# Performance work log

Measured on AMD Instinct MI355X. Metric: run time of the kernel, lower is better.

The kernel has to match this reference:

```python
import jax, jax.numpy as jnp
import numpy as np

N_NODES = 100000
N_EDGES = 1600000
NEG_SLOPE = 0.2  # DGL GATConv default leaky_relu slope
BN_EPS = 1e-5


def setup_inputs() -> dict:
    key = jax.random.key(0)
    ks = jax.random.split(key, 10)
    feats = jax.random.normal(ks[0], (N_NODES, 128), dtype=jnp.float32)
    src = jax.random.randint(ks[1], (N_EDGES,), 0, N_NODES, dtype=jnp.int64)
    dst = jax.random.randint(ks[2], (N_EDGES,), 0, N_NODES, dtype=jnp.int64)
    fc_w = jax.random.normal(ks[3], (256, 128), dtype=jnp.float32) * 0.05   # H*D x in_feats
    attn_l = jax.random.normal(ks[4], (4, 64), dtype=jnp.float32) * 0.05
    attn_r = jax.random.normal(ks[5], (4, 64), dtype=jnp.float32) * 0.05
    res_w = jax.random.normal(ks[6], (256, 128), dtype=jnp.float32) * 0.05  # residual projection
    bias = jax.random.normal(ks[7], (4, 64), dtype=jnp.float32) * 0.05
    gamma = jnp.ones((64,), dtype=jnp.float32)
    beta = jnp.zeros((64,), dtype=jnp.float32)
    return {"feats": feats, "src": src, "dst": dst, "fc_w": fc_w,
            "attn_l": attn_l, "attn_r": attn_r, "res_w": res_w,
            "bias": bias, "gamma": gamma, "beta": beta}


def reference(feats, src, dst, fc_w, attn_l, attn_r, res_w, bias, gamma, beta):
    N = feats.shape[0]
    H, D = attn_l.shape
    # projected features [N, H, D] (feat_drop is identity in eval mode)
    h = (feats @ fc_w.T).reshape(N, H, D)
    # per-node attention logits [N, H]
    el = jnp.sum(h * attn_l[None], axis=-1)
    er = jnp.sum(h * attn_r[None], axis=-1)
    # edge logits, leaky relu
    e = el[src] + er[dst]                       # [E, H]
    e = jnp.where(e > 0, e, NEG_SLOPE * e)
    # numerically stable segment softmax over incoming edges of each dst node
    m = jax.ops.segment_max(e, dst, num_segments=N)       # [N, H]
    ex = jnp.exp(e - m[dst])                               # [E, H]
    s = jax.ops.segment_sum(ex, dst, num_segments=N)       # [N, H]
    alpha = ex / s[dst]                                    # [E, H]
    # weighted message aggregation: scatter-add alpha * h_src into dst
    msg = h[src] * alpha[:, :, None]                       # [E, H, D]
    rst = jax.ops.segment_sum(msg, dst, num_segments=N)    # [N, H, D]
    # residual projection + bias + activation (elu)
    res = (feats @ res_w.T).reshape(N, H, D)
    rst = jax.nn.elu(rst + res + bias[None])
    # mean over heads -> [N, D]
    out = rst.mean(axis=1)
    # BatchNorm1d (training stats: biased variance over the node/batch axis)
    mu = out.mean(axis=0)
    var = out.var(axis=0)
    return (out - mu) * jax.lax.rsqrt(var + BN_EPS) * gamma + beta
```

## Files before the change

### kernel.cpp

```cpp
#include <hip/hip_runtime.h>

#define N_NODES 100000
#define N_PAD   100096
#define N_EDGES 1600000
#define NEG_SLOPE 0.2f
#define BN_EPS 1e-5f

typedef __attribute__((ext_vector_type(8))) short short8;
typedef __attribute__((ext_vector_type(4))) float floatx4;

static const size_t OFF_AB   = 0;
static const size_t OFF_BB   = 25624576;
static const size_t OFF_H    = 25755648;
static const size_t OFF_RES  = 76955648;
static const size_t OFF_EL   = 128155648;
static const size_t OFF_ER   = 129755648;
static const size_t OFF_DEG  = 131355648;
static const size_t OFF_RS   = 131755648;
static const size_t OFF_CUR  = 132155664;
static const size_t OFF_ESRC = 132555664;
static const size_t OFF_BS   = 138955664;
static const size_t OFF_BN   = 138956176;

__device__ __forceinline__ unsigned short f2bf(float x) {
  unsigned int u = __float_as_uint(x);
  unsigned int r = (u + 0x7fffu + ((u >> 16) & 1u)) >> 16;
  return (unsigned short)r;
}
__device__ __forceinline__ float bf2f(unsigned short u) {
  return __uint_as_float(((unsigned int)u) << 16);
}

__global__ __launch_bounds__(256) void k_pre(
    const float* __restrict__ feats, const float* __restrict__ fc_w,
    const float* __restrict__ res_w, const int* __restrict__ dst,
    unsigned short* __restrict__ Ab, unsigned short* __restrict__ Bb,
    int* __restrict__ deg)
{
  const int b = blockIdx.x;
  if (b < 6256) {
    int c = b * 256 + threadIdx.x;
    int r = c >> 4, j = c & 15;
    unsigned short v[8];
    if (r < N_NODES) {
      const float* p = feats + (size_t)r * 128 + j * 8;
      float4 a = *(const float4*)p, bb = *(const float4*)(p + 4);
      v[0]=f2bf(a.x); v[1]=f2bf(a.y); v[2]=f2bf(a.z); v[3]=f2bf(a.w);
      v[4]=f2bf(bb.x); v[5]=f2bf(bb.y); v[6]=f2bf(bb.z); v[7]=f2bf(bb.w);
    } else {
      for (int i = 0; i < 8; i++) v[i] = 0;
    }
    size_t idx = (size_t)(r >> 7) * 2048 + ((r >> 4) & 7) * 256 + (j >> 2) * 64
               + (r & 15) + 16 * (j & 3);
    *(short8*)(Ab + idx * 8) = *(short8*)v;
  } else if (b < 12506) {
    int e = (b - 6256) * 256 + threadIdx.x;
    if (e < N_EDGES) atomicAdd(&deg[dst[e]], 1);
  } else {
    int c = (b - 12506) * 256 + threadIdx.x;
    int n = c >> 4, j = c & 15;
    const float* W = (n < 256) ? (fc_w + (size_t)n * 128) : (res_w + (size_t)(n - 256) * 128);
    const float* p = W + j * 8;
    float4 a = *(const float4*)p, bb = *(const float4*)(p + 4);
    unsigned short v[8];
    v[0]=f2bf(a.x); v[1]=f2bf(a.y); v[2]=f2bf(a.z); v[3]=f2bf(a.w);
    v[4]=f2bf(bb.x); v[5]=f2bf(bb.y); v[6]=f2bf(bb.z); v[7]=f2bf(bb.w);
    size_t idx = (size_t)(n >> 7) * 2048 + ((n >> 4) & 7) * 256 + (j >> 2) * 64
               + (n & 15) + 16 * (j & 3);
    *(short8*)(Bb + idx * 8) = *(short8*)v;
  }
}

__global__ __launch_bounds__(256) void k_mm(
    const unsigned short* __restrict__ Ab, const unsigned short* __restrict__ Bb,
    const float* __restrict__ bias, const float* __restrict__ attn_l,
    const float* __restrict__ attn_r,
    unsigned short* __restrict__ hbuf, unsigned short* __restrict__ resbuf,
    float* __restrict__ el, float* __restrict__ er)
{
  __shared__ unsigned short sA[16384];
  const int tid = threadIdx.x;
  const int w = tid >> 6, L = tid & 63;
  const int blk = blockIdx.x, nb = blockIdx.y;

  {
    const unsigned short* ga = Ab + (size_t)blk * 16384;
    #pragma unroll
    for (int i = 0; i < 8; i++) {
      int off = (i * 256 + w * 64) * 8;
      __builtin_amdgcn_global_load_lds(
          (const __attribute__((address_space(1))) unsigned int*)(ga + off + L * 8),
          (__attribute__((address_space(3))) unsigned int*)(sA + off),
          16, 0, 0);
    }
  }
  const int mh = w & 1, nh = w >> 1;
  floatx4 acc[4][4] = {};
  __syncthreads();

  const unsigned short* gb = Bb + ((size_t)nb * 2048 + nh * 4 * 256) * 8 + L * 8;
  #pragma unroll
  for (int s = 0; s < 4; s++) {
    short8 a[4], b[4];
    #pragma unroll
    for (int t = 0; t < 4; t++)
      a[t] = *(const short8*)(sA + ((mh * 4 + t) * 256 + s * 64 + L) * 8);
    #pragma unroll
    for (int t = 0; t < 4; t++)
      b[t] = *(const short8*)(gb + ((size_t)t * 256 + s * 64) * 8);
    #pragma unroll
    for (int mt = 0; mt < 4; mt++)
      #pragma unroll
      for (int nt = 0; nt < 4; nt++)
        acc[mt][nt] = __builtin_amdgcn_mfma_f32_16x16x32_bf16(a[mt], b[nt], acc[mt][nt], 0, 0, 0);
  }

  const int q = L >> 4, cn = L & 15;
  const int r0 = blk * 128 + mh * 64;
  if (nb < 2) {
    const int head = nb * 2 + nh;
    const int col0 = nb * 128 + nh * 64;
    float al[4], ar[4];
    #pragma unroll
    for (int nt = 0; nt < 4; nt++) {
      al[nt] = attn_l[head * 64 + nt * 16 + cn];
      ar[nt] = attn_r[head * 64 + nt * 16 + cn];
    }
    #pragma unroll
    for (int mt = 0; mt < 4; mt++)
      #pragma unroll
      for (int r = 0; r < 4; r++) {
        const int row = r0 + mt * 16 + q * 4 + r;
        float pl = 0.f, pr = 0.f;
        #pragma unroll
        for (int nt = 0; nt < 4; nt++) {
          pl = fmaf(acc[mt][nt][r], al[nt], pl);
          pr = fmaf(acc[mt][nt][r], ar[nt], pr);
        }
        #pragma unroll
        for (int o = 1; o < 16; o <<= 1) {
          pl += __shfl_xor(pl, o, 64);
          pr += __shfl_xor(pr, o, 64);
        }
        if (row < N_NODES) {
          #pragma unroll
          for (int nt = 0; nt < 4; nt++)
            hbuf[(size_t)row * 256 + col0 + nt * 16 + cn] = f2bf(acc[mt][nt][r]);
          if (cn == 0) {
            el[row * 4 + head] = pl;
            er[row * 4 + head] = pr;
          }
        }
      }
  } else {
    const int rc0 = (nb - 2) * 128 + nh * 64;
    #pragma unroll
    for (int mt = 0; mt < 4; mt++)
      #pragma unroll
      for (int r = 0; r < 4; r++) {
        const int row = r0 + mt * 16 + q * 4 + r;
        if (row < N_NODES)
          #pragma unroll
          for (int nt = 0; nt < 4; nt++) {
            float v = acc[mt][nt][r] + bias[rc0 + nt * 16 + cn];
            resbuf[(size_t)row * 256 + rc0 + nt * 16 + cn] = f2bf(v);
          }
      }
  }
}

__global__ __launch_bounds__(256) void k_scan1(const int* __restrict__ deg,
                                               int* __restrict__ rs, int* __restrict__ bsums)
{
  __shared__ int tmp[256];
  const int t = threadIdx.x;
  const int base = blockIdx.x * 1024 + t * 4;
  int v0 = 0, v1 = 0, v2 = 0, v3 = 0;
  if (base + 0 < N_NODES) v0 = deg[base + 0];
  if (base + 1 < N_NODES) v1 = deg[base + 1];
  if (base + 2 < N_NODES) v2 = deg[base + 2];
  if (base + 3 < N_NODES) v3 = deg[base + 3];
  const int tsum = v0 + v1 + v2 + v3;
  tmp[t] = tsum;
  __syncthreads();
  for (int o = 1; o < 256; o <<= 1) {
    int x = (t >= o) ? tmp[t - o] : 0;
    __syncthreads();
    tmp[t] += x;
    __syncthreads();
  }
  const int excl = tmp[t] - tsum;
  if (base + 0 < N_NODES) rs[base + 0] = excl;
  if (base + 1 < N_NODES) rs[base + 1] = excl + v0;
  if (base + 2 < N_NODES) rs[base + 2] = excl + v0 + v1;
  if (base + 3 < N_NODES) rs[base + 3] = excl + v0 + v1 + v2;
  if (t == 255) bsums[blockIdx.x] = tmp[t];
}

__global__ __launch_bounds__(256) void k_scan3(int* __restrict__ rs,
                                               const int* __restrict__ bsums,
                                               int* __restrict__ cursor)
{
  __shared__ int sb[128];
  const int t = threadIdx.x;
  int raw = 0;
  if (t < 128) { raw = (t < 98) ? bsums[t] : 0; sb[t] = raw; }
  __syncthreads();
  for (int o = 1; o < 128; o <<= 1) {
    int x = (t >= o && t < 128) ? sb[t - o] : 0;
    __syncthreads();
    if (t < 128) sb[t] += x;
    __syncthreads();
  }
  if (t < 128) sb[t] -= raw;
  __syncthreads();
  const int i = blockIdx.x * 256 + t;
  if (i < N_NODES) {
    int v = rs[i] + sb[i >> 10];
    rs[i] = v;
    cursor[i] = v;
  } else if (i == N_NODES) {
    rs[N_NODES] = N_EDGES;
  }
}

__global__ __launch_bounds__(256) void k_scatter(const int* __restrict__ src,
                                                 const int* __restrict__ dst,
                                                 int* __restrict__ cursor,
                                                 int* __restrict__ esrc)
{
  int e = blockIdx.x * 256 + threadIdx.x;
  if (e >= N_EDGES) return;
  int d = dst[e];
  int pos = atomicAdd(&cursor[d], 1);
  esrc[pos] = src[e];
}

__global__ __launch_bounds__(256) void k_agg(
    const unsigned short* __restrict__ hbuf, const unsigned short* __restrict__ resbuf,
    const float* __restrict__ el, const float* __restrict__ er,
    const int* __restrict__ rs, const int* __restrict__ esrc,
    float* __restrict__ out, float* __restrict__ bn)
{
  const int lane = threadIdx.x & 63;
  const int head = lane >> 4;
  const int waveG = blockIdx.x * 4 + (threadIdx.x >> 6);
  const int nW = gridDim.x * 4;
  float4 s4 = make_float4(0.f, 0.f, 0.f, 0.f);
  float4 q4 = make_float4(0.f, 0.f, 0.f, 0.f);
  for (int n = waveG; n < N_NODES; n += nW) {
    const int nu = __builtin_amdgcn_readfirstlane(n);
    const int p0 = __builtin_amdgcn_readfirstlane(rs[nu]);
    const int p1 = __builtin_amdgcn_readfirstlane(rs[nu + 1]);
    const float ern = er[nu * 4 + head];
    float4 acc = make_float4(0.f, 0.f, 0.f, 0.f);
    float ssum = 0.f;
    int p = p0;
    for (; p + 8 <= p1; p += 8) {
      int sn[8];
      #pragma unroll
      for (int i = 0; i < 8; i++) sn[i] = esrc[p + i];
      float ev[8];
      #pragma unroll
      for (int i = 0; i < 8; i++) ev[i] = el[sn[i] * 4 + head];
      ushort4 hv[8];
      #pragma unroll
      for (int i = 0; i < 8; i++)
        hv[i] = *(const ushort4*)(hbuf + (size_t)sn[i] * 256 + lane * 4);
      #pragma unroll
      for (int i = 0; i < 8; i++) {
        float e = ev[i] + ern;
        e = (e > 0.f) ? e : NEG_SLOPE * e;
        const float wgt = __expf(e);
        ssum += wgt;
        acc.x = fmaf(wgt, bf2f(hv[i].x), acc.x);
        acc.y = fmaf(wgt, bf2f(hv[i].y), acc.y);
        acc.z = fmaf(wgt, bf2f(hv[i].z), acc.z);
        acc.w = fmaf(wgt, bf2f(hv[i].w), acc.w);
      }
    }
    for (; p + 4 <= p1; p += 4) {
      int sn[4];
      #pragma unroll
      for (int i = 0; i < 4; i++) sn[i] = esrc[p + i];
      float ev[4];
      #pragma unroll
      for (int i = 0; i < 4; i++) ev[i] = el[sn[i] * 4 + head];
      ushort4 hv[4];
      #pragma unroll
      for (int i = 0; i < 4; i++)
        hv[i] = *(const ushort4*)(hbuf + (size_t)sn[i] * 256 + lane * 4);
      #pragma unroll
      for (int i = 0; i < 4; i++) {
        float e = ev[i] + ern;
        e = (e > 0.f) ? e : NEG_SLOPE * e;
        const float wgt = __expf(e);
        ssum += wgt;
        acc.x = fmaf(wgt, bf2f(hv[i].x), acc.x);
        acc.y = fmaf(wgt, bf2f(hv[i].y), acc.y);
        acc.z = fmaf(wgt, bf2f(hv[i].z), acc.z);
        acc.w = fmaf(wgt, bf2f(hv[i].w), acc.w);
      }
    }
    for (; p < p1; p++) {
      int sn = esrc[p];
      float e = el[sn * 4 + head] + ern;
      e = (e > 0.f) ? e : NEG_SLOPE * e;
      const float wgt = __expf(e);
      ssum += wgt;
      const ushort4 hv4 = *(const ushort4*)(hbuf + (size_t)sn * 256 + lane * 4);
      acc.x = fmaf(wgt, bf2f(hv4.x), acc.x);
      acc.y = fmaf(wgt, bf2f(hv4.y), acc.y);
      acc.z = fmaf(wgt, bf2f(hv4.z), acc.z);
      acc.w = fmaf(wgt, bf2f(hv4.w), acc.w);
    }
    const float inv = (p1 > p0) ? (1.0f / ssum) : 0.f;
    const ushort4 rv4 = *(const ushort4*)(resbuf + (size_t)nu * 256 + lane * 4);
    float4 v;
    v.x = fmaf(acc.x, inv, bf2f(rv4.x));
    v.y = fmaf(acc.y, inv, bf2f(rv4.y));
    v.z = fmaf(acc.z, inv, bf2f(rv4.z));
    v.w = fmaf(acc.w, inv, bf2f(rv4.w));
    v.x = (v.x > 0.f) ? v.x : (__expf(v.x) - 1.f);
    v.y = (v.y > 0.f) ? v.y : (__expf(v.y) - 1.f);
    v.z = (v.z > 0.f) ? v.z : (__expf(v.z) - 1.f);
    v.w = (v.w > 0.f) ? v.w : (__expf(v.w) - 1.f);
    v.x += __shfl_xor(v.x, 16, 64);  v.x += __shfl_xor(v.x, 32, 64);
    v.y += __shfl_xor(v.y, 16, 64);  v.y += __shfl_xor(v.y, 32, 64);
    v.z += __shfl_xor(v.z, 16, 64);  v.z += __shfl_xor(v.z, 32, 64);
    v.w += __shfl_xor(v.w, 16, 64);  v.w += __shfl_xor(v.w, 32, 64);
    if (lane < 16) {
      v.x *= 0.25f; v.y *= 0.25f; v.z *= 0.25f; v.w *= 0.25f;
      *(float4*)(out + (size_t)nu * 64 + lane * 4) = v;
      s4.x += v.x; s4.y += v.y; s4.z += v.z; s4.w += v.w;
      q4.x += v.x * v.x; q4.y += v.y * v.y; q4.z += v.z * v.z; q4.w += v.w * v.w;
    }
  }
  __shared__ float lsum[64], lsq[64];
  if (threadIdx.x < 64) { lsum[threadIdx.x] = 0.f; lsq[threadIdx.x] = 0.f; }
  __syncthreads();
  if (lane < 16) {
    atomicAdd(&lsum[lane * 4 + 0], s4.x);  atomicAdd(&lsq[lane * 4 + 0], q4.x);
    atomicAdd(&lsum[lane * 4 + 1], s4.y);  atomicAdd(&lsq[lane * 4 + 1], q4.y);
    atomicAdd(&lsum[lane * 4 + 2], s4.z);  atomicAdd(&lsq[lane * 4 + 2], q4.z);
    atomicAdd(&lsum[lane * 4 + 3], s4.w);  atomicAdd(&lsq[lane * 4 + 3], q4.w);
  }
  __syncthreads();
  if (threadIdx.x < 64) {
    atomicAdd(&bn[threadIdx.x], lsum[threadIdx.x]);
    atomicAdd(&bn[64 + threadIdx.x], lsq[threadIdx.x]);
  }
}

__global__ __launch_bounds__(256) void k_bn_apply(float* __restrict__ out,
                                                  const float* __restrict__ bn,
                                                  const float* __restrict__ gamma,
                                                  const float* __restrict__ beta)
{
  __shared__ float sc[64], sh[64];
  const int t = threadIdx.x;
  if (t < 64) {
    float mean = bn[t] * (1.0f / N_NODES);
    float var = bn[64 + t] * (1.0f / N_NODES) - mean * mean;
    float s = gamma[t] * rsqrtf(var + BN_EPS);
    sc[t] = s;
    sh[t] = beta[t] - mean * s;
  }
  __syncthreads();
  const int i = blockIdx.x * 256 + t;
  if (i >= N_NODES * 16) return;
  const int d0 = (i & 15) * 4;
  float4 v = *(float4*)(out + (size_t)i * 4);
  v.x = fmaf(v.x, sc[d0 + 0], sh[d0 + 0]);
  v.y = fmaf(v.y, sc[d0 + 1], sh[d0 + 1]);
  v.z = fmaf(v.z, sc[d0 + 2], sh[d0 + 2]);
  v.w = fmaf(v.w, sc[d0 + 3], sh[d0 + 3]);
  *(float4*)(out + (size_t)i * 4) = v;
}

extern "C" void kernel_launch(void* const* d_in, const int* in_sizes, int n_in,
                              void* d_out, int out_size, void* d_ws, size_t ws_size,
                              hipStream_t stream)
{
  const float* feats  = (const float*)d_in[0];
  const int*   src    = (const int*)d_in[1];
  const int*   dst    = (const int*)d_in[2];
  const float* fc_w   = (const float*)d_in[3];
  const float* attn_l = (const float*)d_in[4];
  const float* attn_r = (const float*)d_in[5];
  const float* res_w  = (const float*)d_in[6];
  const float* bias   = (const float*)d_in[7];
  const float* gamma  = (const float*)d_in[8];
  const float* beta   = (const float*)d_in[9];

  char* ws = (char*)d_ws;
  unsigned short* Ab     = (unsigned short*)(ws + OFF_AB);
  unsigned short* Bb     = (unsigned short*)(ws + OFF_BB);
  unsigned short* hbuf   = (unsigned short*)(ws + OFF_H);
  unsigned short* resbuf = (unsigned short*)(ws + OFF_RES);
  float* elb    = (float*)(ws + OFF_EL);
  float* erb    = (float*)(ws + OFF_ER);
  int*   deg    = (int*)(ws + OFF_DEG);
  int*   rsb    = (int*)(ws + OFF_RS);
  int*   curb   = (int*)(ws + OFF_CUR);
  int*   esrc   = (int*)(ws + OFF_ESRC);
  int*   bsums  = (int*)(ws + OFF_BS);
  float* bnb    = (float*)(ws + OFF_BN);
  float* outp   = (float*)d_out;

  hipMemsetAsync(deg, 0, N_NODES * sizeof(int), stream);
  hipMemsetAsync(bnb, 0, 128 * sizeof(float), stream);

  k_pre<<<12538, 256, 0, stream>>>(feats, fc_w, res_w, dst, Ab, Bb, deg);
  k_mm<<<dim3(782, 4), 256, 0, stream>>>(Ab, Bb, bias, attn_l, attn_r,
                                         hbuf, resbuf, elb, erb);
  k_scan1<<<98, 256, 0, stream>>>(deg, rsb, bsums);
  k_scan3<<<391, 256, 0, stream>>>(rsb, bsums, curb);
  k_scatter<<<6250, 256, 0, stream>>>(src, dst, curb, esrc);
  k_agg<<<2048, 256, 0, stream>>>(hbuf, resbuf, elb, erb, rsb, esrc, outp, bnb);
  k_bn_apply<<<6250, 256, 0, stream>>>(outp, bnb, gamma, beta);
}
```

Baseline: 534.4 us.

## Pad CSR rows to multiples of eight and software-pipeline edge gathers across nodes

Each node's edge list is padded to a multiple of eight, with padding entries pointing at a dummy node whose el is -1e30 and whose features are zero. Each wave now processes a contiguous range of nodes as one continuous edge stream, using a three-stage register pipeline that prefetches esrc, el and h for the next batches while computing the current one. This targets gather latency and the scalar tail loops of the old per-node loop. In exchange it adds padded-edge work, more register pressure (launch bounds set to 4), and relies on exp(-1e30) underflowing to exactly zero.

```diff
diff --git a/kernel.cpp b/kernel.cpp
--- a/kernel.cpp
+++ b/kernel.cpp
@@ -1,7 +1,6 @@
 #include <hip/hip_runtime.h>
 
 #define N_NODES 100000
-#define N_PAD   100096
 #define N_EDGES 1600000
 #define NEG_SLOPE 0.2f
 #define BN_EPS 1e-5f
@@ -12,15 +11,15 @@
 static const size_t OFF_AB   = 0;
 static const size_t OFF_BB   = 25624576;
 static const size_t OFF_H    = 25755648;
-static const size_t OFF_RES  = 76955648;
-static const size_t OFF_EL   = 128155648;
-static const size_t OFF_ER   = 129755648;
-static const size_t OFF_DEG  = 131355648;
-static const size_t OFF_RS   = 131755648;
-static const size_t OFF_CUR  = 132155664;
-static const size_t OFF_ESRC = 132555664;
-static const size_t OFF_BS   = 138955664;
-static const size_t OFF_BN   = 138956176;
+static const size_t OFF_RES  = 76956672;
+static const size_t OFF_EL   = 128156672;
+static const size_t OFF_ER   = 129757184;
+static const size_t OFF_DEG  = 131357184;
+static const size_t OFF_RS   = 131757184;
+static const size_t OFF_CUR  = 132157568;
+static const size_t OFF_ESRC = 132557568;
+static const size_t OFF_BS   = 142157568;
+static const size_t OFF_BN   = 142158080;
 
 __device__ __forceinline__ unsigned short f2bf(float x) {
   unsigned int u = __float_as_uint(x);
@@ -35,7 +34,8 @@
     const float* __restrict__ feats, const float* __restrict__ fc_w,
     const float* __restrict__ res_w, const int* __restrict__ dst,
     unsigned short* __restrict__ Ab, unsigned short* __restrict__ Bb,
-    int* __restrict__ deg)
+    int* __restrict__ deg, unsigned short* __restrict__ hbuf,
+    float* __restrict__ el)
 {
   const int b = blockIdx.x;
   if (b < 6256) {
@@ -56,7 +56,7 @@
   } else if (b < 12506) {
     int e = (b - 6256) * 256 + threadIdx.x;
     if (e < N_EDGES) atomicAdd(&deg[dst[e]], 1);
-  } else {
+  } else if (b < 12538) {
     int c = (b - 12506) * 256 + threadIdx.x;
     int n = c >> 4, j = c & 15;
     const float* W = (n < 256) ? (fc_w + (size_t)n * 128) : (res_w + (size_t)(n - 256) * 128);
@@ -68,6 +68,10 @@
     size_t idx = (size_t)(n >> 7) * 2048 + ((n >> 4) & 7) * 256 + (j >> 2) * 64
                + (n & 15) + 16 * (j & 3);
     *(short8*)(Bb + idx * 8) = *(short8*)v;
+  } else {
+    const int t = threadIdx.x;
+    hbuf[(size_t)N_NODES * 256 + t] = 0;
+    if (t < 4) el[N_NODES * 4 + t] = -1e30f;
   }
 }
 
@@ -176,10 +180,10 @@
   const int t = threadIdx.x;
   const int base = blockIdx.x * 1024 + t * 4;
   int v0 = 0, v1 = 0, v2 = 0, v3 = 0;
-  if (base + 0 < N_NODES) v0 = deg[base + 0];
-  if (base + 1 < N_NODES) v1 = deg[base + 1];
-  if (base + 2 < N_NODES) v2 = deg[base + 2];
-  if (base + 3 < N_NODES) v3 = deg[base + 3];
+  if (base + 0 < N_NODES) v0 = (deg[base + 0] + 7) & ~7;
+  if (base + 1 < N_NODES) v1 = (deg[base + 1] + 7) & ~7;
+  if (base + 2 < N_NODES) v2 = (deg[base + 2] + 7) & ~7;
+  if (base + 3 < N_NODES) v3 = (deg[base + 3] + 7) & ~7;
   const int tsum = v0 + v1 + v2 + v3;
   tmp[t] = tsum;
   __syncthreads();
@@ -199,7 +203,9 @@
 
 __global__ __launch_bounds__(256) void k_scan3(int* __restrict__ rs,
                                                const int* __restrict__ bsums,
-                                               int* __restrict__ cursor)
+                                               int* __restrict__ cursor,
+                                               const int* __restrict__ deg,
+                                               int* __restrict__ esrc)
 {
   __shared__ int sb[128];
   const int t = threadIdx.x;
@@ -219,8 +225,10 @@
     int v = rs[i] + sb[i >> 10];
     rs[i] = v;
     cursor[i] = v;
-  } else if (i == N_NODES) {
-    rs[N_NODES] = N_EDGES;
+    const int d = deg[i];
+    const int pd = (d + 7) & ~7;
+    for (int j = d; j < pd; j++) esrc[v + j] = N_NODES;
+    if (i == N_NODES - 1) rs[N_NODES] = v + pd;
   }
 }
 
@@ -236,7 +244,7 @@
   esrc[pos] = src[e];
 }
 
-__global__ __launch_bounds__(256) void k_agg(
+__global__ __launch_bounds__(256, 4) void k_agg(
     const unsigned short* __restrict__ hbuf, const unsigned short* __restrict__ resbuf,
     const float* __restrict__ el, const float* __restrict__ er,
     const int* __restrict__ rs, const int* __restrict__ esrc,
@@ -244,98 +252,128 @@
 {
   const int lane = threadIdx.x & 63;
   const int head = lane >> 4;
-  const int waveG = blockIdx.x * 4 + (threadIdx.x >> 6);
+  const int wid = blockIdx.x * 4 + (threadIdx.x >> 6);
   const int nW = gridDim.x * 4;
   float4 s4 = make_float4(0.f, 0.f, 0.f, 0.f);
   float4 q4 = make_float4(0.f, 0.f, 0.f, 0.f);
-  for (int n = waveG; n < N_NODES; n += nW) {
-    const int nu = __builtin_amdgcn_readfirstlane(n);
-    const int p0 = __builtin_amdgcn_readfirstlane(rs[nu]);
-    const int p1 = __builtin_amdgcn_readfirstlane(rs[nu + 1]);
-    const float ern = er[nu * 4 + head];
+
+  const int n0 = (int)(((long long)wid * N_NODES) / nW);
+  const int n1 = (int)(((long long)(wid + 1) * N_NODES) / nW);
+
+  if (n0 < n1) {
+    int nu = __builtin_amdgcn_readfirstlane(n0);
+    int nend = __builtin_amdgcn_readfirstlane(rs[nu + 1]);
+    const int p_beg = __builtin_amdgcn_readfirstlane(rs[n0]);
+    const int p_end = __builtin_amdgcn_readfirstlane(rs[n1]);
+    float ern = er[nu * 4 + head];
+    float ern_nx = (nu + 1 < N_NODES) ? er[(nu + 1) * 4 + head] : 0.f;
+    ushort4 rv_cur = *(const ushort4*)(resbuf + (size_t)nu * 256 + lane * 4);
+
     float4 acc = make_float4(0.f, 0.f, 0.f, 0.f);
     float ssum = 0.f;
-    int p = p0;
-    for (; p + 8 <= p1; p += 8) {
-      int sn[8];
-      #pragma unroll
-      for (int i = 0; i < 8; i++) sn[i] = esrc[p + i];
-      float ev[8];
-      #pragma unroll
-      for (int i = 0; i < 8; i++) ev[i] = el[sn[i] * 4 + head];
-      ushort4 hv[8];
+
+    auto fin = [&](int nd) {
+      const float inv = (ssum > 0.f) ? (1.0f / ssum) : 0.f;
+      float4 v;
+      v.x = fmaf(acc.x, inv, bf2f(rv_cur.x));
+      v.y = fmaf(acc.y, inv, bf2f(rv_cur.y));
+      v.z = fmaf(acc.z, inv, bf2f(rv_cur.z));
+      v.w = fmaf(acc.w, inv, bf2f(rv_cur.w));
+      v.x = (v.x > 0.f) ? v.x : (__expf(v.x) - 1.f);
+      v.y = (v.y > 0.f) ? v.y : (__expf(v.y) - 1.f);
+      v.z = (v.z > 0.f) ? v.z : (__expf(v.z) - 1.f);
+      v.w = (v.w > 0.f) ? v.w : (__expf(v.w) - 1.f);
+      v.x += __shfl_xor(v.x, 16, 64);  v.x += __shfl_xor(v.x, 32, 64);
+      v.y += __shfl_xor(v.y, 16, 64);  v.y += __shfl_xor(v.y, 32, 64);
+      v.z += __shfl_xor(v.z, 16, 64);  v.z += __shfl_xor(v.z, 32, 64);
+      v.w += __shfl_xor(v.w, 16, 64);  v.w += __shfl_xor(v.w, 32, 64);
+      if (lane < 16) {
+        v.x *= 0.25f; v.y *= 0.25f; v.z *= 0.25f; v.w *= 0.25f;
+        *(float4*)(out + (size_t)nd * 64 + lane * 4) = v;
+        s4.x += v.x; s4.y += v.y; s4.z += v.z; s4.w += v.w;
+        q4.x += v.x * v.x; q4.y += v.y * v.y; q4.z += v.z * v.z; q4.w += v.w * v.w;
+      }
+    };
+
+    int sn0[8], sn1[8], sn2[8];
+    float ev0[8], ev1[8], ev2[8];
+    ushort4 hv0[8], hv1[8], hv2[8];
+
+    int p = p_beg;
+    if (p < p_end) {
+      #pragma unroll
+      for (int i = 0; i < 8; i++) sn0[i] = __builtin_amdgcn_readfirstlane(esrc[p + i]);
+      #pragma unroll
+      for (int i = 0; i < 8; i++) ev0[i] = el[sn0[i] * 4 + head];
       #pragma unroll
       for (int i = 0; i < 8; i++)
-        hv[i] = *(const ushort4*)(hbuf + (size_t)sn[i] * 256 + lane * 4);
+        hv0[i] = *(const ushort4*)(hbuf + (size_t)sn0[i] * 256 + lane * 4);
+    }
+    if (p + 8 < p_end) {
+      #pragma unroll
+      for (int i = 0; i < 8; i++) sn1[i] = __builtin_amdgcn_readfirstlane(esrc[p + 8 + i]);
+      #pragma unroll
+      for (int i = 0; i < 8; i++) ev1[i] = el[sn1[i] * 4 + head];
+      #pragma unroll
+      for (int i = 0; i < 8; i++)
+        hv1[i] = *(const ushort4*)(hbuf + (size_t)sn1[i] * 256 + lane * 4);
+    }
+    if (p + 16 < p_end) {
+      #pragma unroll
+      for (int i = 0; i < 8; i++) sn2[i] = __builtin_amdgcn_readfirstlane(esrc[p + 16 + i]);
+    }
+
+    auto STEP = [&](int pc, float (&evc)[8], ushort4 (&hvc)[8],
+                    float (&evg)[8], ushort4 (&hvg)[8],
+                    int (&sng)[8], int (&snl)[8]) {
+      if (pc + 16 < p_end) {
+        #pragma unroll
+        for (int i = 0; i < 8; i++) evg[i] = el[sng[i] * 4 + head];
+        #pragma unroll
+        for (int i = 0; i < 8; i++)
+          hvg[i] = *(const ushort4*)(hbuf + (size_t)sng[i] * 256 + lane * 4);
+      }
+      if (pc + 24 < p_end) {
+        #pragma unroll
+        for (int i = 0; i < 8; i++)
+          snl[i] = __builtin_amdgcn_readfirstlane(esrc[pc + 24 + i]);
+      }
+      while (pc == nend) {
+        fin(nu);
+        acc = make_float4(0.f, 0.f, 0.f, 0.f); ssum = 0.f;
+        nu++;
+        nend = __builtin_amdgcn_readfirstlane(rs[nu + 1]);
+        ern = ern_nx;
+        rv_cur = *(const ushort4*)(resbuf + (size_t)nu * 256 + lane * 4);
+        const int nn = nu + 1;
+        ern_nx = (nn < N_NODES) ? er[nn * 4 + head] : 0.f;
+      }
       #pragma unroll
       for (int i = 0; i < 8; i++) {
-        float e = ev[i] + ern;
+        float e = evc[i] + ern;
         e = (e > 0.f) ? e : NEG_SLOPE * e;
-        const float wgt = __expf(e);
-        ssum += wgt;
-        acc.x = fmaf(wgt, bf2f(hv[i].x), acc.x);
-        acc.y = fmaf(wgt, bf2f(hv[i].y), acc.y);
-        acc.z = fmaf(wgt, bf2f(hv[i].z), acc.z);
-        acc.w = fmaf(wgt, bf2f(hv[i].w), acc.w);
-      }
-    }
-    for (; p + 4 <= p1; p += 4) {
-      int sn[4];
-      #pragma unroll
-      for (int i = 0; i < 4; i++) sn[i] = esrc[p + i];
-      float ev[4];
-      #pragma unroll
-      for (int i = 0; i < 4; i++) ev[i] = el[sn[i] * 4 + head];
-      ushort4 hv[4];
-      #pragma unroll
-      for (int i = 0; i < 4; i++)
-        hv[i] = *(const ushort4*)(hbuf + (size_t)sn[i] * 256 + lane * 4);
-      #pragma unroll
-      for (int i = 0; i < 4; i++) {
-        float e = ev[i] + ern;
-        e = (e > 0.f) ? e : NEG_SLOPE * e;
-        const float wgt = __expf(e);
-        ssum += wgt;
-        acc.x = fmaf(wgt, bf2f(hv[i].x), acc.x);
-        acc.y = fmaf(wgt, bf2f(hv[i].y), acc.y);
-        acc.z = fmaf(wgt, bf2f(hv[i].z), acc.z);
-        acc.w = fmaf(wgt, bf2f(hv[i].w), acc.w);
-      }
-    }
-    for (; p < p1; p++) {
-      int sn = esrc[p];
-      float e = el[sn * 4 + head] + ern;
-      e = (e > 0.f) ? e : NEG_SLOPE * e;
-      const float wgt = __expf(e);
-      ssum += wgt;
-      const ushort4 hv4 = *(const ushort4*)(hbuf + (size_t)sn * 256 + lane * 4);
-      acc.x = fmaf(wgt, bf2f(hv4.x), acc.x);
-      acc.y = fmaf(wgt, bf2f(hv4.y), acc.y);
-      acc.z = fmaf(wgt, bf2f(hv4.z), acc.z);
-      acc.w = fmaf(wgt, bf2f(hv4.w), acc.w);
-    }
-    const float inv = (p1 > p0) ? (1.0f / ssum) : 0.f;
-    const ushort4 rv4 = *(const ushort4*)(resbuf + (size_t)nu * 256 + lane * 4);
-    float4 v;
-    v.x = fmaf(acc.x, inv, bf2f(rv4.x));
-    v.y = fmaf(acc.y, inv, bf2f(rv4.y));
-    v.z = fmaf(acc.z, inv, bf2f(rv4.z));
-    v.w = fmaf(acc.w, inv, bf2f(rv4.w));
-    v.x = (v.x > 0.f) ? v.x : (__expf(v.x) - 1.f);
-    v.y = (v.y > 0.f) ? v.y : (__expf(v.y) - 1.f);
-    v.z = (v.z > 0.f) ? v.z : (__expf(v.z) - 1.f);
-    v.w = (v.w > 0.f) ? v.w : (__expf(v.w) - 1.f);
-    v.x += __shfl_xor(v.x, 16, 64);  v.x += __shfl_xor(v.x, 32, 64);
-    v.y += __shfl_xor(v.y, 16, 64);  v.y += __shfl_xor(v.y, 32, 64);
-    v.z += __shfl_xor(v.z, 16, 64);  v.z += __shfl_xor(v.z, 32, 64);
-    v.w += __shfl_xor(v.w, 16, 64);  v.w += __shfl_xor(v.w, 32, 64);
-    if (lane < 16) {
-      v.x *= 0.25f; v.y *= 0.25f; v.z *= 0.25f; v.w *= 0.25f;
-      *(float4*)(out + (size_t)nu * 64 + lane * 4) = v;
-      s4.x += v.x; s4.y += v.y; s4.z += v.z; s4.w += v.w;
-      q4.x += v.x * v.x; q4.y += v.y * v.y; q4.z += v.z * v.z; q4.w += v.w * v.w;
-    }
-  }
+        const float w = __expf(e);
+        ssum += w;
+        acc.x = fmaf(w, bf2f(hvc[i].x), acc.x);
+        acc.y = fmaf(w, bf2f(hvc[i].y), acc.y);
+        acc.z = fmaf(w, bf2f(hvc[i].z), acc.z);
+        acc.w = fmaf(w, bf2f(hvc[i].w), acc.w);
+      }
+    };
+
+    while (p < p_end) {
+      STEP(p, ev0, hv0, ev2, hv2, sn2, sn0); p += 8; if (p >= p_end) break;
+      STEP(p, ev1, hv1, ev0, hv0, sn0, sn1); p += 8; if (p >= p_end) break;
+      STEP(p, ev2, hv2, ev1, hv1, sn1, sn2); p += 8;
+    }
+    while (nu < n1) {
+      fin(nu);
+      acc = make_float4(0.f, 0.f, 0.f, 0.f); ssum = 0.f;
+      nu++;
+      if (nu < n1) rv_cur = *(const ushort4*)(resbuf + (size_t)nu * 256 + lane * 4);
+    }
+  }
+
   __shared__ float lsum[64], lsq[64];
   if (threadIdx.x < 64) { lsum[threadIdx.x] = 0.f; lsq[threadIdx.x] = 0.f; }
   __syncthreads();
@@ -411,11 +449,11 @@
   hipMemsetAsync(deg, 0, N_NODES * sizeof(int), stream);
   hipMemsetAsync(bnb, 0, 128 * sizeof(float), stream);
 
-  k_pre<<<12538, 256, 0, stream>>>(feats, fc_w, res_w, dst, Ab, Bb, deg);
+  k_pre<<<12539, 256, 0, stream>>>(feats, fc_w, res_w, dst, Ab, Bb, deg, hbuf, elb);
   k_mm<<<dim3(782, 4), 256, 0, stream>>>(Ab, Bb, bias, attn_l, attn_r,
                                          hbuf, resbuf, elb, erb);
   k_scan1<<<98, 256, 0, stream>>>(deg, rsb, bsums);
-  k_scan3<<<391, 256, 0, stream>>>(rsb, bsums, curb);
+  k_scan3<<<391, 256, 0, stream>>>(rsb, bsums, curb, deg, esrc);
   k_scatter<<<6250, 256, 0, stream>>>(src, dst, curb, esrc);
   k_agg<<<2048, 256, 0, stream>>>(hbuf, resbuf, elb, erb, rsb, esrc, outp, bnb);
   k_bn_apply<<<6250, 256, 0, stream>>>(outp, bnb, gamma, beta);
```

New measurement: 722.9 us. +35.3%, slower.
